# Optimization experiments

Measured on AMD Instinct MI355X. Metric: run time of the kernel, lower is better.

## Reference

```python
import jax, jax.numpy as jnp
import numpy as np

HIDDEN = 128
VOCAB = 100000
NUM_CLASSES = 5
N_LEAVES = 65536  # complete binary tree -> 2*N_LEAVES-1 = 131071 nodes


def setup_inputs() -> dict:
    key = jax.random.key(0)
    ks = jax.random.split(key, 24)
    H, C = HIDDEN, NUM_CLASSES

    def w(k, o, i):
        return (jax.random.normal(k, (o, i), jnp.float32) / np.sqrt(i)).astype(jnp.float32)

    def b(k, o):
        return jax.random.normal(k, (o,), jnp.float32) * 0.01

    inp = {
        "leaf_tokens": jax.random.randint(ks[0], (N_LEAVES,), 0, VOCAB, dtype=jnp.int64 if jax.config.jax_enable_x64 else jnp.int32).astype(jnp.int32),
        "node_labels": jax.random.randint(ks[1], (2 * N_LEAVES - 1,), 0, NUM_CLASSES).astype(jnp.int32),
        "embed": jax.random.uniform(ks[2], (VOCAB, H), jnp.float32, -0.5 / H, 0.5 / H),
        "W_i_w": w(ks[3], H, H), "W_i_b": b(ks[4], H),
        "W_o_w": w(ks[5], H, H), "W_o_b": b(ks[6], H),
        "W_u_w": w(ks[7], H, H), "W_u_b": b(ks[8], H),
        "U_i_w": w(ks[9], H, 2 * H), "U_i_b": b(ks[10], H),
        "U_o_w": w(ks[11], H, 2 * H), "U_o_b": b(ks[12], H),
        "U_u_w": w(ks[13], H, 2 * H), "U_u_b": b(ks[14], H),
        "F1_w": w(ks[15], H, H), "F1_b": b(ks[16], H),
        "F2_w": w(ks[17], H, H), "F2_b": b(ks[18], H),
        "out_w": w(ks[19], C, H), "out_b": b(ks[20], C),
    }
    return inp


def reference(leaf_tokens, node_labels, embed,
              W_i_w, W_i_b, W_o_w, W_o_b, W_u_w, W_u_b,
              U_i_w, U_i_b, U_o_w, U_o_b, U_u_w, U_u_b,
              F1_w, F1_b, F2_w, F2_b, out_w, out_b):
    def aff(x, wgt, bias):
        return x @ wgt.T + bias

    # ---- leaves: x = embed[token]; c = sigmoid(W_i x) * tanh(W_u x) ----
    x = embed[leaf_tokens]                          # [L, H]
    i = jax.nn.sigmoid(aff(x, W_i_w, W_i_b))
    o = jax.nn.sigmoid(aff(x, W_o_w, W_o_b))
    u = jnp.tanh(aff(x, W_u_w, W_u_b))
    c = i * u
    h = o * jnp.tanh(c)
    outs = [aff(h, out_w, out_b)]                   # dropout is identity at eval

    # ---- internal levels, bottom-up, all same-depth nodes batched ----
    n_levels = int(np.log2(N_LEAVES))
    for _ in range(n_levels):
        hl, hr = h[0::2], h[1::2]                   # [n/2, H] each
        cl, cr = c[0::2], c[1::2]
        xc = jnp.concatenate([hl, hr], axis=1)      # [n/2, 2H]
        i = jax.nn.sigmoid(aff(xc, U_i_w, U_i_b))
        o = jax.nn.sigmoid(aff(xc, U_o_w, U_o_b))
        u = jnp.tanh(aff(xc, U_u_w, U_u_b))
        f1 = jax.nn.sigmoid(aff(hl, F1_w, F1_b))
        f2 = jax.nn.sigmoid(aff(hr, F2_w, F2_b))
        c = i * u + f1 * cl + f2 * cr
        h = o * jnp.tanh(c)
        outs.append(aff(h, out_w, out_b))

    outputs = jnp.concatenate(outs, axis=0)         # [2L-1, num_classes]
    return outputs, node_labels
```

## Files before the change

### kernel.cpp

```cpp
#include <hip/hip_runtime.h>
#include <hip/hip_bf16.h>
#include <math.h>

#define H    128
#define NC   5
#define LPI  264
#define LPL  136
#define HPAD 136
#define CBP  132

typedef unsigned short ushort_t;
using frag_ab = __attribute__((ext_vector_type(8))) short;
using frag_cd = __attribute__((ext_vector_type(4))) float;

__device__ __forceinline__ float fsig(float x) { return 1.0f / (1.0f + __expf(-x)); }
__device__ __forceinline__ float ftanh_(float x) {
    float e = __expf(-2.0f * fabsf(x));
    float t = (1.0f - e) / (1.0f + e);
    return copysignf(t, x);
}
__device__ __forceinline__ ushort_t f2bf(float f) {
    __hip_bfloat16 b = __float2bfloat16(f);
    return *reinterpret_cast<ushort_t*>(&b);
}

__global__ __launch_bounds__(256) void prep_weights(
    const float* __restrict__ Ui, const float* __restrict__ Uo, const float* __restrict__ Uu,
    const float* __restrict__ F1, const float* __restrict__ F2,
    const float* __restrict__ Wi, const float* __restrict__ Wo, const float* __restrict__ Wu,
    const float* __restrict__ Wout,
    ushort_t* __restrict__ Wf, ushort_t* __restrict__ Wlf, ushort_t* __restrict__ Woutf)
{
    int e = blockIdx.x * 256 + threadIdx.x;
    if (e < 131072) {
        int kc = e >> 12, rem = e & 4095;
        int n = rem >> 3, j7 = rem & 7;
        int k = kc * 8 + j7;
        int g = n >> 7, jc = n & 127;
        float v;
        if (g == 0)      v = Ui[jc * 256 + k];
        else if (g == 1) v = Uo[jc * 256 + k];
        else if (g == 2) v = Uu[jc * 256 + k];
        else             v = (k < 128) ? F1[jc * 128 + k] : F2[jc * 128 + k - 128];
        Wf[e] = f2bf(v);
    } else if (e < 180224) {
        int e2 = e - 131072;
        int kc = e2 / 3072, rem = e2 % 3072;
        int n = rem >> 3, j7 = rem & 7;
        int k = kc * 8 + j7;
        int g = n >> 7, jc = n & 127;
        float v = (g == 0) ? Wi[jc * 128 + k] : (g == 1) ? Wo[jc * 128 + k] : Wu[jc * 128 + k];
        Wlf[e2] = f2bf(v);
    } else {
        int e3 = e - 180224;
        int kcq = e3 >> 7, rem = e3 & 127;
        int col = rem >> 3, j7 = rem & 7;
        int k = kcq * 8 + j7;
        float v = (col < NC) ? Wout[col * H + k] : 0.0f;
        Woutf[e3] = f2bf(v);
    }
}

__global__ __launch_bounds__(512) void leaf_l1_mfma(
    const int* __restrict__ tokens, const float* __restrict__ embed,
    const ushort_t* __restrict__ Wlf, const ushort_t* __restrict__ Wf,
    const ushort_t* __restrict__ Woutf,
    const float* __restrict__ bi, const float* __restrict__ bo, const float* __restrict__ bu,
    const float* __restrict__ bui, const float* __restrict__ buo, const float* __restrict__ buu,
    const float* __restrict__ bf1, const float* __restrict__ bf2,
    const float* __restrict__ bout,
    const int* __restrict__ labels, float* __restrict__ lab_out,
    ushort_t* __restrict__ h1_out, float* __restrict__ c1_out,
    float* __restrict__ out_leaf, float* __restrict__ out_l1)
{
    __shared__ ushort_t xs [32 * LPL];
    __shared__ ushort_t hh [32 * HPAD];
    __shared__ float    cbL[32 * CBP];
    __shared__ ushort_t xs2[16 * LPI];
    const int tid = threadIdx.x;
    const int node_base  = blockIdx.x * 32;
    const int node1_base = blockIdx.x * 16;

    if (tid < 64) {
        int id = blockIdx.x * 64 + tid;
        if (id < 131071) lab_out[id] = (float)labels[id];
    }

    {
        int m = tid >> 4, kp = (tid & 15) * 8;
        const float* src = embed + (size_t)tokens[node_base + m] * H + kp;
        ushort_t tmp[8];
#pragma unroll
        for (int v = 0; v < 2; ++v) {
            float4 f = *(const float4*)(src + v * 4);
            tmp[v * 4 + 0] = f2bf(f.x); tmp[v * 4 + 1] = f2bf(f.y);
            tmp[v * 4 + 2] = f2bf(f.z); tmp[v * 4 + 3] = f2bf(f.w);
        }
        *(uint4*)&xs[m * LPL + kp] = *(uint4*)tmp;
    }

    const int w = tid >> 6, lane = tid & 63;
    const int mA = lane & 15, q = lane >> 4, nlane = lane & 15;

    frag_ab wb[4];
#pragma unroll
    for (int kc8 = 0; kc8 < 4; ++kc8)
        wb[kc8] = *(const frag_ab*)&Woutf[(((kc8 * 4 + q) * 16) + nlane) * 8];
    float bout_l = (nlane < NC) ? bout[nlane] : 0.0f;

    const int jt = w;
    const int j = jt * 16 + nlane;
    __syncthreads();

    frag_ab a[2][4];
#pragma unroll
    for (int t = 0; t < 2; ++t)
#pragma unroll
        for (int kc8 = 0; kc8 < 4; ++kc8)
            a[t][kc8] = *(const frag_ab*)&xs[(t * 16 + mA) * LPL + (kc8 * 4 + q) * 8];

    {
        frag_cd acc[3][2];
#pragma unroll
        for (int g = 0; g < 3; ++g)
#pragma unroll
            for (int t = 0; t < 2; ++t) acc[g][t] = (frag_cd){0.f, 0.f, 0.f, 0.f};
#pragma unroll
        for (int kc8 = 0; kc8 < 4; ++kc8) {
            int kcq = kc8 * 4 + q;
            const ushort_t* wp = &Wlf[((size_t)kcq * 384 + jt * 16 + nlane) * 8];
#pragma unroll
            for (int g = 0; g < 3; ++g) {
                frag_ab b = *(const frag_ab*)(wp + (size_t)g * H * 8);
                acc[g][0] = __builtin_amdgcn_mfma_f32_16x16x32_bf16(a[0][kc8], b, acc[g][0], 0, 0, 0);
                acc[g][1] = __builtin_amdgcn_mfma_f32_16x16x32_bf16(a[1][kc8], b, acc[g][1], 0, 0, 0);
            }
        }
        float bi_ = bi[j], bo_ = bo[j], bu_ = bu[j];
#pragma unroll
        for (int t = 0; t < 2; ++t)
#pragma unroll
            for (int r = 0; r < 4; ++r) {
                int nloc = t * 16 + q * 4 + r;
                float i_ = fsig(acc[0][t][r] + bi_);
                float o_ = fsig(acc[1][t][r] + bo_);
                float u_ = ftanh_(acc[2][t][r] + bu_);
                float c_ = i_ * u_;
                float h_ = o_ * ftanh_(c_);
                cbL[nloc * CBP + j] = c_;
                ushort_t hb = f2bf(h_);
                hh[nloc * HPAD + j] = hb;
                xs2[(nloc >> 1) * LPI + (nloc & 1) * H + j] = hb;
            }
    }
    __syncthreads();

    frag_ab a1[8];
#pragma unroll
    for (int kc8 = 0; kc8 < 8; ++kc8)
        a1[kc8] = *(const frag_ab*)&xs2[mA * LPI + (kc8 * 4 + q) * 8];

    if (w < 2) {
        frag_cd ha = (frag_cd){0.f, 0.f, 0.f, 0.f};
#pragma unroll
        for (int kc8 = 0; kc8 < 4; ++kc8) {
            frag_ab av = *(const frag_ab*)&hh[(w * 16 + mA) * HPAD + (kc8 * 4 + q) * 8];
            ha = __builtin_amdgcn_mfma_f32_16x16x32_bf16(av, wb[kc8], ha, 0, 0, 0);
        }
        if (nlane < NC) {
#pragma unroll
            for (int r = 0; r < 4; ++r)
                out_leaf[(size_t)(node_base + w * 16 + q * 4 + r) * NC + nlane] = ha[r] + bout_l;
        }
    }
    __syncthreads();

    {
        frag_cd acc[5];
#pragma unroll
        for (int g = 0; g < 5; ++g) acc[g] = (frag_cd){0.f, 0.f, 0.f, 0.f};
#pragma unroll
        for (int kc8 = 0; kc8 < 8; ++kc8) {
            int kcq = kc8 * 4 + q;
            const ushort_t* wp = &Wf[((size_t)kcq * 512 + jt * 16 + nlane) * 8];
#pragma unroll
            for (int g = 0; g < 4; ++g) {
                frag_ab b = *(const frag_ab*)(wp + (size_t)g * H * 8);
                int gi = (g < 3) ? g : (kc8 < 4 ? 3 : 4);
                acc[gi] = __builtin_amdgcn_mfma_f32_16x16x32_bf16(a1[kc8], b, acc[gi], 0, 0, 0);
            }
        }
        float bi_ = bui[j], bo_ = buo[j], bu_ = buu[j], b1_ = bf1[j], b2_ = bf2[j];
#pragma unroll
        for (int r = 0; r < 4; ++r) {
            int nloc = q * 4 + r;
            int nd = node1_base + nloc;
            float i_  = fsig(acc[0][r] + bi_);
            float o_  = fsig(acc[1][r] + bo_);
            float u_  = ftanh_(acc[2][r] + bu_);
            float f1_ = fsig(acc[3][r] + b1_);
            float f2_ = fsig(acc[4][r] + b2_);
            float cl = cbL[(2 * nloc) * CBP + j];
            float cr = cbL[(2 * nloc + 1) * CBP + j];
            float c_ = fmaf(i_, u_, fmaf(f1_, cl, f2_ * cr));
            float h_ = o_ * ftanh_(c_);
            c1_out[(size_t)nd * H + j] = c_;
            ushort_t hb = f2bf(h_);
            h1_out[(size_t)nd * H + j] = hb;
            hh[nloc * HPAD + j] = hb;
        }
    }
    __syncthreads();

    if (w == 0) {
        frag_cd ha = (frag_cd){0.f, 0.f, 0.f, 0.f};
#pragma unroll
        for (int kc8 = 0; kc8 < 4; ++kc8) {
            frag_ab av = *(const frag_ab*)&hh[mA * HPAD + (kc8 * 4 + q) * 8];
            ha = __builtin_amdgcn_mfma_f32_16x16x32_bf16(av, wb[kc8], ha, 0, 0, 0);
        }
        if (nlane < NC) {
#pragma unroll
            for (int r = 0; r < 4; ++r)
                out_l1[(size_t)(node1_base + q * 4 + r) * NC + nlane] = ha[r] + bout_l;
        }
    }
}

__global__ __launch_bounds__(512) void pair_level_mfma(
    const ushort_t* __restrict__ h_prev, const float* __restrict__ c_prev,
    const ushort_t* __restrict__ Wf, const ushort_t* __restrict__ Woutf,
    const float* __restrict__ bui, const float* __restrict__ buo, const float* __restrict__ buu,
    const float* __restrict__ bf1, const float* __restrict__ bf2,
    const float* __restrict__ bout,
    ushort_t* __restrict__ hB_out, float* __restrict__ cB_out,
    float* __restrict__ out_A, float* __restrict__ out_B)
{
    __shared__ ushort_t xs [32 * LPI];
    __shared__ ushort_t hh [32 * HPAD];
    __shared__ float    cbL[32 * CBP];
    __shared__ ushort_t xs2[16 * LPI];
    const int tid = threadIdx.x;
    const int node_baseA = blockIdx.x * 32;
    const int node_baseB = blockIdx.x * 16;

    {
        int m = tid >> 4, kp = (tid & 15) * 16;
        const uint4* s = (const uint4*)(h_prev +
            ((size_t)2 * (node_baseA + m) + (kp >> 7)) * H + (kp & 127));
        uint4* d = (uint4*)&xs[m * LPI + kp];
        d[0] = s[0]; d[1] = s[1];
    }

    const int w = tid >> 6, lane = tid & 63;
    const int mA = lane & 15, q = lane >> 4, nlane = lane & 15;

    frag_ab wb[4];
#pragma unroll
    for (int kc8 = 0; kc8 < 4; ++kc8)
        wb[kc8] = *(const frag_ab*)&Woutf[(((kc8 * 4 + q) * 16) + nlane) * 8];
    float bout_l = (nlane < NC) ? bout[nlane] : 0.0f;

    const int jt = w;
    const int j = jt * 16 + nlane;
    const float bi_ = bui[j], bo_ = buo[j], bu_ = buu[j], b1_ = bf1[j], b2_ = bf2[j];
    __syncthreads();

    frag_ab a[2][8];
#pragma unroll
    for (int t = 0; t < 2; ++t)
#pragma unroll
        for (int kc8 = 0; kc8 < 8; ++kc8)
            a[t][kc8] = *(const frag_ab*)&xs[(t * 16 + mA) * LPI + (kc8 * 4 + q) * 8];

    {
        frag_cd acc[5][2];
#pragma unroll
        for (int g = 0; g < 5; ++g)
#pragma unroll
            for (int t = 0; t < 2; ++t) acc[g][t] = (frag_cd){0.f, 0.f, 0.f, 0.f};
#pragma unroll
        for (int kc8 = 0; kc8 < 8; ++kc8) {
            int kcq = kc8 * 4 + q;
            const ushort_t* wp = &Wf[((size_t)kcq * 512 + jt * 16 + nlane) * 8];
#pragma unroll
            for (int g = 0; g < 4; ++g) {
                frag_ab b = *(const frag_ab*)(wp + (size_t)g * H * 8);
                int gi = (g < 3) ? g : (kc8 < 4 ? 3 : 4);
                acc[gi][0] = __builtin_amdgcn_mfma_f32_16x16x32_bf16(a[0][kc8], b, acc[gi][0], 0, 0, 0);
                acc[gi][1] = __builtin_amdgcn_mfma_f32_16x16x32_bf16(a[1][kc8], b, acc[gi][1], 0, 0, 0);
            }
        }
#pragma unroll
        for (int t = 0; t < 2; ++t)
#pragma unroll
            for (int r = 0; r < 4; ++r) {
                int nloc = t * 16 + q * 4 + r;
                int nd = node_baseA + nloc;
                float i_  = fsig(acc[0][t][r] + bi_);
                float o_  = fsig(acc[1][t][r] + bo_);
                float u_  = ftanh_(acc[2][t][r] + bu_);
                float f1_ = fsig(acc[3][t][r] + b1_);
                float f2_ = fsig(acc[4][t][r] + b2_);
                float cl = c_prev[((size_t)2 * nd) * H + j];
                float cr = c_prev[((size_t)2 * nd + 1) * H + j];
                float c_ = fmaf(i_, u_, fmaf(f1_, cl, f2_ * cr));
                float h_ = o_ * ftanh_(c_);
                cbL[nloc * CBP + j] = c_;
                ushort_t hb = f2bf(h_);
                hh[nloc * HPAD + j] = hb;
                xs2[(nloc >> 1) * LPI + (nloc & 1) * H + j] = hb;
            }
    }
    __syncthreads();

    frag_ab a1[8];
#pragma unroll
    for (int kc8 = 0; kc8 < 8; ++kc8)
        a1[kc8] = *(const frag_ab*)&xs2[mA * LPI + (kc8 * 4 + q) * 8];

    if (w < 2) {
        frag_cd ha = (frag_cd){0.f, 0.f, 0.f, 0.f};
#pragma unroll
        for (int kc8 = 0; kc8 < 4; ++kc8) {
            frag_ab av = *(const frag_ab*)&hh[(w * 16 + mA) * HPAD + (kc8 * 4 + q) * 8];
            ha = __builtin_amdgcn_mfma_f32_16x16x32_bf16(av, wb[kc8], ha, 0, 0, 0);
        }
        if (nlane < NC) {
#pragma unroll
            for (int r = 0; r < 4; ++r)
                out_A[(size_t)(node_baseA + w * 16 + q * 4 + r) * NC + nlane] = ha[r] + bout_l;
        }
    }
    __syncthreads();

    {
        frag_cd acc[5];
#pragma unroll
        for (int g = 0; g < 5; ++g) acc[g] = (frag_cd){0.f, 0.f, 0.f, 0.f};
#pragma unroll
        for (int kc8 = 0; kc8 < 8; ++kc8) {
            int kcq = kc8 * 4 + q;
            const ushort_t* wp = &Wf[((size_t)kcq * 512 + jt * 16 + nlane) * 8];
#pragma unroll
            for (int g = 0; g < 4; ++g) {
                frag_ab b = *(const frag_ab*)(wp + (size_t)g * H * 8);
                int gi = (g < 3) ? g : (kc8 < 4 ? 3 : 4);
                acc[gi] = __builtin_amdgcn_mfma_f32_16x16x32_bf16(a1[kc8], b, acc[gi], 0, 0, 0);
            }
        }
#pragma unroll
        for (int r = 0; r < 4; ++r) {
            int nloc = q * 4 + r;
            int nd = node_baseB + nloc;
            float i_  = fsig(acc[0][r] + bi_);
            float o_  = fsig(acc[1][r] + bo_);
            float u_  = ftanh_(acc[2][r] + bu_);
            float f1_ = fsig(acc[3][r] + b1_);
            float f2_ = fsig(acc[4][r] + b2_);
            float cl = cbL[(2 * nloc) * CBP + j];
            float cr = cbL[(2 * nloc + 1) * CBP + j];
            float c_ = fmaf(i_, u_, fmaf(f1_, cl, f2_ * cr));
            float h_ = o_ * ftanh_(c_);
            cB_out[(size_t)nd * H + j] = c_;
            ushort_t hb = f2bf(h_);
            hB_out[(size_t)nd * H + j] = hb;
            hh[nloc * HPAD + j] = hb;
        }
    }
    __syncthreads();

    if (w == 0) {
        frag_cd ha = (frag_cd){0.f, 0.f, 0.f, 0.f};
#pragma unroll
        for (int kc8 = 0; kc8 < 4; ++kc8) {
            frag_ab av = *(const frag_ab*)&hh[mA * HPAD + (kc8 * 4 + q) * 8];
            ha = __builtin_amdgcn_mfma_f32_16x16x32_bf16(av, wb[kc8], ha, 0, 0, 0);
        }
        if (nlane < NC) {
#pragma unroll
            for (int r = 0; r < 4; ++r)
                out_B[(size_t)(node_baseB + q * 4 + r) * NC + nlane] = ha[r] + bout_l;
        }
    }
}

__global__ __launch_bounds__(512) void tail_mfma(
    const ushort_t* __restrict__ h_prev, const float* __restrict__ c_prev,
    const ushort_t* __restrict__ Wf, const ushort_t* __restrict__ Woutf,
    const float* __restrict__ bui, const float* __restrict__ buo, const float* __restrict__ buu,
    const float* __restrict__ bf1, const float* __restrict__ bf2,
    const float* __restrict__ bout, float* __restrict__ out)
{
    __shared__ ushort_t xsA[64 * LPI];
    __shared__ ushort_t xsB[32 * LPI];
    __shared__ float    cbA[64 * H];
    __shared__ float    cbB[32 * H];
    __shared__ ushort_t hh[64 * HPAD];
    const int tid = threadIdx.x;
    const int w = tid >> 6, lane = tid & 63;
    const int mA = lane & 15, q = lane >> 4, nlane = lane & 15;

    {
        int m = tid >> 3, kp = (tid & 7) * 32;
        const uint4* s = (const uint4*)(h_prev + ((size_t)2 * m + (kp >> 7)) * H + (kp & 127));
        uint4* d = (uint4*)&xsA[m * LPI + kp];
#pragma unroll
        for (int i = 0; i < 4; ++i) d[i] = s[i];
    }

    frag_ab wb[4];
#pragma unroll
    for (int kc8 = 0; kc8 < 4; ++kc8)
        wb[kc8] = *(const frag_ab*)&Woutf[(((kc8 * 4 + q) * 16) + nlane) * 8];
    float bout_l = (nlane < NC) ? bout[nlane] : 0.0f;

    const int jt = w;
    const int j = jt * 16 + nlane;
    const float bi_ = bui[j], bo_ = buo[j], bu_ = buu[j], b1_ = bf1[j], b2_ = bf2[j];

    float* outp = out;
    for (int lev = 0; lev < 7; ++lev) {
        const int N = 64 >> lev;
        const int ntiles = (N + 15) >> 4;
        ushort_t* xs_cur = (lev & 1) ? xsB : xsA;
        ushort_t* xs_nxt = (lev & 1) ? xsA : xsB;
        float*    cb_out = (lev & 1) ? cbB : cbA;
        const float* cb_in = (lev & 1) ? cbA : cbB;
        __syncthreads();

        for (int t = 0; t < ntiles; ++t) {
            frag_cd acc[5];
#pragma unroll
            for (int g = 0; g < 5; ++g) acc[g] = (frag_cd){0.f, 0.f, 0.f, 0.f};
#pragma unroll
            for (int kc8 = 0; kc8 < 8; ++kc8) {
                int kcq = kc8 * 4 + q;
                frag_ab av = *(const frag_ab*)&xs_cur[(t * 16 + mA) * LPI + kcq * 8];
                const ushort_t* wp = &Wf[((size_t)kcq * 512 + jt * 16 + nlane) * 8];
#pragma unroll
                for (int g = 0; g < 4; ++g) {
                    frag_ab b = *(const frag_ab*)(wp + (size_t)g * H * 8);
                    int gi = (g < 3) ? g : (kc8 < 4 ? 3 : 4);
                    acc[gi] = __builtin_amdgcn_mfma_f32_16x16x32_bf16(av, b, acc[gi], 0, 0, 0);
                }
            }
#pragma unroll
            for (int r = 0; r < 4; ++r) {
                int nloc = t * 16 + q * 4 + r;
                if (nloc < N) {
                    float i_  = fsig(acc[0][r] + bi_);
                    float o_  = fsig(acc[1][r] + bo_);
                    float u_  = ftanh_(acc[2][r] + bu_);
                    float f1_ = fsig(acc[3][r] + b1_);
                    float f2_ = fsig(acc[4][r] + b2_);
                    float cl, cr;
                    if (lev == 0) {
                        cl = c_prev[((size_t)2 * nloc) * H + j];
                        cr = c_prev[((size_t)2 * nloc + 1) * H + j];
                    } else {
                        cl = cb_in[(2 * nloc) * H + j];
                        cr = cb_in[(2 * nloc + 1) * H + j];
                    }
                    float c_ = fmaf(i_, u_, fmaf(f1_, cl, f2_ * cr));
                    float h_ = o_ * ftanh_(c_);
                    cb_out[nloc * H + j] = c_;
                    ushort_t hb = f2bf(h_);
                    hh[nloc * HPAD + j] = hb;
                    xs_nxt[(nloc >> 1) * LPI + (nloc & 1) * H + j] = hb;
                }
            }
        }
        __syncthreads();
        if (w < ntiles) {
            frag_cd ha = (frag_cd){0.f, 0.f, 0.f, 0.f};
#pragma unroll
            for (int kc8 = 0; kc8 < 4; ++kc8) {
                frag_ab av = *(const frag_ab*)&hh[(w * 16 + mA) * HPAD + (kc8 * 4 + q) * 8];
                ha = __builtin_amdgcn_mfma_f32_16x16x32_bf16(av, wb[kc8], ha, 0, 0, 0);
            }
            if (nlane < NC) {
#pragma unroll
                for (int r = 0; r < 4; ++r) {
                    int nd = w * 16 + q * 4 + r;
                    if (nd < N) outp[(size_t)nd * NC + nlane] = ha[r] + bout_l;
                }
            }
        }
        outp += (size_t)N * NC;
    }
}

extern "C" void kernel_launch(void* const* d_in, const int* in_sizes, int n_in,
                              void* d_out, int out_size, void* d_ws, size_t ws_size,
                              hipStream_t stream)
{
    const int*   tokens = (const int*)d_in[0];
    const int*   labels = (const int*)d_in[1];
    const float* embed  = (const float*)d_in[2];
    const float* Wi = (const float*)d_in[3];  const float* bi  = (const float*)d_in[4];
    const float* Wo = (const float*)d_in[5];  const float* bo  = (const float*)d_in[6];
    const float* Wu = (const float*)d_in[7];  const float* bu  = (const float*)d_in[8];
    const float* Ui = (const float*)d_in[9];  const float* bui = (const float*)d_in[10];
    const float* Uo = (const float*)d_in[11]; const float* buo = (const float*)d_in[12];
    const float* Uu = (const float*)d_in[13]; const float* buu = (const float*)d_in[14];
    const float* F1 = (const float*)d_in[15]; const float* bf1 = (const float*)d_in[16];
    const float* F2 = (const float*)d_in[17]; const float* bf2 = (const float*)d_in[18];
    const float* Wout = (const float*)d_in[19]; const float* bout = (const float*)d_in[20];
    float* out = (float*)d_out;

    const int NL = 65536;
    char* base = (char*)d_ws;
    ushort_t* Wf    = (ushort_t*)(base);
    ushort_t* Wlf   = (ushort_t*)(base + 327680);
    ushort_t* Woutf = (ushort_t*)(base + 425984);
    ushort_t* hA    = (ushort_t*)(base + 430080);
    ushort_t* hB    = (ushort_t*)(base + 17207296);
    float*    cA    = (float*)   (base + 25595904);
    float*    cB    = (float*)   (base + 59150336);

    prep_weights<<<712, 256, 0, stream>>>(Ui, Uo, Uu, F1, F2, Wi, Wo, Wu, Wout,
                                          Wf, Wlf, Woutf);

    const size_t totalN = 2 * (size_t)NL - 1;
    float* lab_out = out + totalN * NC;

    leaf_l1_mfma<<<NL / 32, 512, 0, stream>>>(
        tokens, embed, Wlf, Wf, Woutf, bi, bo, bu, bui, buo, buu, bf1, bf2,
        bout, labels, lab_out, hB, cB, out, out + (size_t)NL * NC);

    size_t off = (size_t)NL * NC + (size_t)(NL / 2) * NC;
    int NA = NL / 4;
    for (int p = 0; p < 4; ++p) {
        const ushort_t* hp = (p & 1) ? hA : hB;
        const float*    cp = (p & 1) ? cA : cB;
        ushort_t* hc = (p & 1) ? hB : hA;
        float*    cc = (p & 1) ? cB : cA;
        pair_level_mfma<<<NA / 32, 512, 0, stream>>>(
            hp, cp, Wf, Woutf, bui, buo, buu, bf1, bf2, bout,
            hc, cc, out + off, out + off + (size_t)NA * NC);
        off += (size_t)NA * NC + (size_t)(NA / 2) * NC;
        NA >>= 2;
    }
    tail_mfma<<<1, 512, 0, stream>>>(hB, cB, Wf, Woutf, bui, buo, buu, bf1, bf2,
                                     bout, out + off);
}
```

Baseline: 259.7 us.

## Fuse four tree levels per launch via block-local subtree kernel

Replaces the four two-level pair kernels with two launches of a subtree kernel. Each block now processes four consecutive tree levels, keeping h and c in shared memory between levels. This removes two launches and the global round-trips of intermediate h/c state. In exchange, the upper levels leave many warps idle, the grids are small (512 and 32 blocks), and the per-tile accumulator loop is no longer unrolled across two tiles.

```diff
diff --git a/kernel.cpp b/kernel.cpp
--- a/kernel.cpp
+++ b/kernel.cpp
@@ -227,28 +227,28 @@
     }
 }
 
-__global__ __launch_bounds__(512) void pair_level_mfma(
+__global__ __launch_bounds__(512) void subtree_mfma(
     const ushort_t* __restrict__ h_prev, const float* __restrict__ c_prev,
     const ushort_t* __restrict__ Wf, const ushort_t* __restrict__ Woutf,
     const float* __restrict__ bui, const float* __restrict__ buo, const float* __restrict__ buu,
     const float* __restrict__ bf1, const float* __restrict__ bf2,
     const float* __restrict__ bout,
-    ushort_t* __restrict__ hB_out, float* __restrict__ cB_out,
-    float* __restrict__ out_A, float* __restrict__ out_B)
+    ushort_t* __restrict__ h_out, float* __restrict__ c_out,
+    float* __restrict__ out_base)
 {
-    __shared__ ushort_t xs [32 * LPI];
+    __shared__ ushort_t xsA[32 * LPI];
+    __shared__ ushort_t xsB[16 * LPI];
+    __shared__ float    cbA[32 * CBP];
+    __shared__ float    cbB[16 * CBP];
     __shared__ ushort_t hh [32 * HPAD];
-    __shared__ float    cbL[32 * CBP];
-    __shared__ ushort_t xs2[16 * LPI];
     const int tid = threadIdx.x;
-    const int node_baseA = blockIdx.x * 32;
-    const int node_baseB = blockIdx.x * 16;
+    const int NB  = gridDim.x;
 
     {
         int m = tid >> 4, kp = (tid & 15) * 16;
         const uint4* s = (const uint4*)(h_prev +
-            ((size_t)2 * (node_baseA + m) + (kp >> 7)) * H + (kp & 127));
-        uint4* d = (uint4*)&xs[m * LPI + kp];
+            ((size_t)2 * (blockIdx.x * 32 + m) + (kp >> 7)) * H + (kp & 127));
+        uint4* d = (uint4*)&xsA[m * LPI + kp];
         d[0] = s[0]; d[1] = s[1];
     }
 
@@ -264,124 +264,83 @@
     const int jt = w;
     const int j = jt * 16 + nlane;
     const float bi_ = bui[j], bo_ = buo[j], bu_ = buu[j], b1_ = bf1[j], b2_ = bf2[j];
-    __syncthreads();
-
-    frag_ab a[2][8];
-#pragma unroll
-    for (int t = 0; t < 2; ++t)
-#pragma unroll
-        for (int kc8 = 0; kc8 < 8; ++kc8)
-            a[t][kc8] = *(const frag_ab*)&xs[(t * 16 + mA) * LPI + (kc8 * 4 + q) * 8];
-
-    {
-        frag_cd acc[5][2];
-#pragma unroll
-        for (int g = 0; g < 5; ++g)
-#pragma unroll
-            for (int t = 0; t < 2; ++t) acc[g][t] = (frag_cd){0.f, 0.f, 0.f, 0.f};
-#pragma unroll
-        for (int kc8 = 0; kc8 < 8; ++kc8) {
-            int kcq = kc8 * 4 + q;
-            const ushort_t* wp = &Wf[((size_t)kcq * 512 + jt * 16 + nlane) * 8];
-#pragma unroll
-            for (int g = 0; g < 4; ++g) {
-                frag_ab b = *(const frag_ab*)(wp + (size_t)g * H * 8);
-                int gi = (g < 3) ? g : (kc8 < 4 ? 3 : 4);
-                acc[gi][0] = __builtin_amdgcn_mfma_f32_16x16x32_bf16(a[0][kc8], b, acc[gi][0], 0, 0, 0);
-                acc[gi][1] = __builtin_amdgcn_mfma_f32_16x16x32_bf16(a[1][kc8], b, acc[gi][1], 0, 0, 0);
-            }
-        }
-#pragma unroll
-        for (int t = 0; t < 2; ++t)
+
+    size_t out_off = 0;
+    for (int lev = 0; lev < 4; ++lev) {
+        const int N = 32 >> lev;
+        const int ntiles = (N + 15) >> 4;
+        const int gbase = blockIdx.x * N;
+        ushort_t* xs_cur = (lev & 1) ? xsB : xsA;
+        ushort_t* xs_nxt = (lev & 1) ? xsA : xsB;
+        float*    cb_out = (lev & 1) ? cbB : cbA;
+        const float* cb_in = (lev & 1) ? cbA : cbB;
+        __syncthreads();
+
+        for (int t = 0; t < ntiles; ++t) {
+            frag_cd acc[5];
+#pragma unroll
+            for (int g = 0; g < 5; ++g) acc[g] = (frag_cd){0.f, 0.f, 0.f, 0.f};
+#pragma unroll
+            for (int kc8 = 0; kc8 < 8; ++kc8) {
+                int kcq = kc8 * 4 + q;
+                frag_ab av = *(const frag_ab*)&xs_cur[(t * 16 + mA) * LPI + kcq * 8];
+                const ushort_t* wp = &Wf[((size_t)kcq * 512 + jt * 16 + nlane) * 8];
+#pragma unroll
+                for (int g = 0; g < 4; ++g) {
+                    frag_ab b = *(const frag_ab*)(wp + (size_t)g * H * 8);
+                    int gi = (g < 3) ? g : (kc8 < 4 ? 3 : 4);
+                    acc[gi] = __builtin_amdgcn_mfma_f32_16x16x32_bf16(av, b, acc[gi], 0, 0, 0);
+                }
+            }
 #pragma unroll
             for (int r = 0; r < 4; ++r) {
                 int nloc = t * 16 + q * 4 + r;
-                int nd = node_baseA + nloc;
-                float i_  = fsig(acc[0][t][r] + bi_);
-                float o_  = fsig(acc[1][t][r] + bo_);
-                float u_  = ftanh_(acc[2][t][r] + bu_);
-                float f1_ = fsig(acc[3][t][r] + b1_);
-                float f2_ = fsig(acc[4][t][r] + b2_);
-                float cl = c_prev[((size_t)2 * nd) * H + j];
-                float cr = c_prev[((size_t)2 * nd + 1) * H + j];
-                float c_ = fmaf(i_, u_, fmaf(f1_, cl, f2_ * cr));
-                float h_ = o_ * ftanh_(c_);
-                cbL[nloc * CBP + j] = c_;
-                ushort_t hb = f2bf(h_);
-                hh[nloc * HPAD + j] = hb;
-                xs2[(nloc >> 1) * LPI + (nloc & 1) * H + j] = hb;
-            }
-    }
-    __syncthreads();
-
-    frag_ab a1[8];
-#pragma unroll
-    for (int kc8 = 0; kc8 < 8; ++kc8)
-        a1[kc8] = *(const frag_ab*)&xs2[mA * LPI + (kc8 * 4 + q) * 8];
-
-    if (w < 2) {
-        frag_cd ha = (frag_cd){0.f, 0.f, 0.f, 0.f};
-#pragma unroll
-        for (int kc8 = 0; kc8 < 4; ++kc8) {
-            frag_ab av = *(const frag_ab*)&hh[(w * 16 + mA) * HPAD + (kc8 * 4 + q) * 8];
-            ha = __builtin_amdgcn_mfma_f32_16x16x32_bf16(av, wb[kc8], ha, 0, 0, 0);
-        }
-        if (nlane < NC) {
-#pragma unroll
-            for (int r = 0; r < 4; ++r)
-                out_A[(size_t)(node_baseA + w * 16 + q * 4 + r) * NC + nlane] = ha[r] + bout_l;
-        }
-    }
-    __syncthreads();
-
-    {
-        frag_cd acc[5];
-#pragma unroll
-        for (int g = 0; g < 5; ++g) acc[g] = (frag_cd){0.f, 0.f, 0.f, 0.f};
-#pragma unroll
-        for (int kc8 = 0; kc8 < 8; ++kc8) {
-            int kcq = kc8 * 4 + q;
-            const ushort_t* wp = &Wf[((size_t)kcq * 512 + jt * 16 + nlane) * 8];
-#pragma unroll
-            for (int g = 0; g < 4; ++g) {
-                frag_ab b = *(const frag_ab*)(wp + (size_t)g * H * 8);
-                int gi = (g < 3) ? g : (kc8 < 4 ? 3 : 4);
-                acc[gi] = __builtin_amdgcn_mfma_f32_16x16x32_bf16(a1[kc8], b, acc[gi], 0, 0, 0);
-            }
-        }
-#pragma unroll
-        for (int r = 0; r < 4; ++r) {
-            int nloc = q * 4 + r;
-            int nd = node_baseB + nloc;
-            float i_  = fsig(acc[0][r] + bi_);
-            float o_  = fsig(acc[1][r] + bo_);
-            float u_  = ftanh_(acc[2][r] + bu_);
-            float f1_ = fsig(acc[3][r] + b1_);
-            float f2_ = fsig(acc[4][r] + b2_);
-            float cl = cbL[(2 * nloc) * CBP + j];
-            float cr = cbL[(2 * nloc + 1) * CBP + j];
-            float c_ = fmaf(i_, u_, fmaf(f1_, cl, f2_ * cr));
-            float h_ = o_ * ftanh_(c_);
-            cB_out[(size_t)nd * H + j] = c_;
-            ushort_t hb = f2bf(h_);
-            hB_out[(size_t)nd * H + j] = hb;
-            hh[nloc * HPAD + j] = hb;
-        }
-    }
-    __syncthreads();
-
-    if (w == 0) {
-        frag_cd ha = (frag_cd){0.f, 0.f, 0.f, 0.f};
-#pragma unroll
-        for (int kc8 = 0; kc8 < 4; ++kc8) {
-            frag_ab av = *(const frag_ab*)&hh[mA * HPAD + (kc8 * 4 + q) * 8];
-            ha = __builtin_amdgcn_mfma_f32_16x16x32_bf16(av, wb[kc8], ha, 0, 0, 0);
-        }
-        if (nlane < NC) {
-#pragma unroll
-            for (int r = 0; r < 4; ++r)
-                out_B[(size_t)(node_baseB + q * 4 + r) * NC + nlane] = ha[r] + bout_l;
-        }
+                if (nloc < N) {
+                    float i_  = fsig(acc[0][r] + bi_);
+                    float o_  = fsig(acc[1][r] + bo_);
+                    float u_  = ftanh_(acc[2][r] + bu_);
+                    float f1_ = fsig(acc[3][r] + b1_);
+                    float f2_ = fsig(acc[4][r] + b2_);
+                    float cl, cr;
+                    if (lev == 0) {
+                        cl = c_prev[((size_t)2 * (gbase + nloc)) * H + j];
+                        cr = c_prev[((size_t)2 * (gbase + nloc) + 1) * H + j];
+                    } else {
+                        cl = cb_in[(2 * nloc) * CBP + j];
+                        cr = cb_in[(2 * nloc + 1) * CBP + j];
+                    }
+                    float c_ = fmaf(i_, u_, fmaf(f1_, cl, f2_ * cr));
+                    float h_ = o_ * ftanh_(c_);
+                    ushort_t hb = f2bf(h_);
+                    hh[nloc * HPAD + j] = hb;
+                    if (lev < 3) {
+                        cb_out[nloc * CBP + j] = c_;
+                        xs_nxt[(nloc >> 1) * LPI + (nloc & 1) * H + j] = hb;
+                    } else {
+                        c_out[(size_t)(gbase + nloc) * H + j] = c_;
+                        h_out[(size_t)(gbase + nloc) * H + j] = hb;
+                    }
+                }
+            }
+        }
+        __syncthreads();
+        if (w < ntiles) {
+            frag_cd ha = (frag_cd){0.f, 0.f, 0.f, 0.f};
+#pragma unroll
+            for (int kc8 = 0; kc8 < 4; ++kc8) {
+                frag_ab av = *(const frag_ab*)&hh[(w * 16 + mA) * HPAD + (kc8 * 4 + q) * 8];
+                ha = __builtin_amdgcn_mfma_f32_16x16x32_bf16(av, wb[kc8], ha, 0, 0, 0);
+            }
+            if (nlane < NC) {
+#pragma unroll
+                for (int r = 0; r < 4; ++r) {
+                    int nd = w * 16 + q * 4 + r;
+                    if (nd < N)
+                        out_base[out_off + (size_t)(gbase + nd) * NC + nlane] = ha[r] + bout_l;
+                }
+            }
+        }
+        out_off += (size_t)NB * N * NC;
     }
 }
 
@@ -529,19 +488,16 @@
         tokens, embed, Wlf, Wf, Woutf, bi, bo, bu, bui, buo, buu, bf1, bf2,
         bout, labels, lab_out, hB, cB, out, out + (size_t)NL * NC);
 
-    size_t off = (size_t)NL * NC + (size_t)(NL / 2) * NC;
-    int NA = NL / 4;
-    for (int p = 0; p < 4; ++p) {
-        const ushort_t* hp = (p & 1) ? hA : hB;
-        const float*    cp = (p & 1) ? cA : cB;
-        ushort_t* hc = (p & 1) ? hB : hA;
-        float*    cc = (p & 1) ? cB : cA;
-        pair_level_mfma<<<NA / 32, 512, 0, stream>>>(
-            hp, cp, Wf, Woutf, bui, buo, buu, bf1, bf2, bout,
-            hc, cc, out + off, out + off + (size_t)NA * NC);
-        off += (size_t)NA * NC + (size_t)(NA / 2) * NC;
-        NA >>= 2;
-    }
+    size_t off = (size_t)(NL + NL / 2) * NC;
+
+    subtree_mfma<<<512, 512, 0, stream>>>(
+        hB, cB, Wf, Woutf, bui, buo, buu, bf1, bf2, bout, hA, cA, out + off);
+    off += (size_t)(16384 + 8192 + 4096 + 2048) * NC;
+
+    subtree_mfma<<<32, 512, 0, stream>>>(
+        hA, cA, Wf, Woutf, bui, buo, buu, bf1, bf2, bout, hB, cB, out + off);
+    off += (size_t)(1024 + 512 + 256 + 128) * NC;
+
     tail_mfma<<<1, 512, 0, stream>>>(hB, cB, Wf, Woutf, bui, buo, buu, bf1, bf2,
                                      bout, out + off);
 }
```

Result: faster. 252.3 us (-2.8%).
